# Kernel tuning notes

Measured on AMD Instinct MI355X. Metric: run time of the kernel, lower is better.

Reference implementation:

```python
import jax, jax.numpy as jnp
import numpy as np

B, N_C, N_T, D, DF = 16, 2048, 1024, 2, 2
K, E_OBS = 16, 4
H, DH = 4, 16
F = H * DH  # 64-dim node features (embed_all output)


def setup_inputs() -> dict:
    key = jax.random.key(0)
    ks = jax.random.split(key, 16)
    r = lambda i, shape: jax.random.normal(ks[i], shape, jnp.float32) * 0.05
    d_in = E_OBS + D + DF  # obs(4) + s(2) + f(2) = 8
    return dict(
        s_ctx=jax.random.normal(ks[0], (B, N_C, D), jnp.float32),
        f_ctx=jax.random.normal(ks[1], (B, N_C, DF), jnp.float32),
        s_test=jax.random.normal(ks[2], (B, N_T, D), jnp.float32),
        emb_obs=r(3, (2, E_OBS)),
        W1=r(4, (d_in, 256)), b1=jnp.zeros((256,), jnp.float32),
        W2=r(5, (256, 128)), b2=jnp.zeros((128,), jnp.float32),
        W3=r(6, (128, F)), b3=jnp.zeros((F,), jnp.float32),
        ln_g=jnp.ones((F,), jnp.float32), ln_b=jnp.zeros((F,), jnp.float32),
        Wg=r(7, (F, F)),
        a_src=r(8, (H, DH)), a_dst=r(9, (H, DH)),
        We=r(10, (D, H)), be=jnp.zeros((H,), jnp.float32),
        H1=r(11, (F, 256)), c1=jnp.zeros((256,), jnp.float32),
        H2=r(12, (256, 64)), c2=jnp.zeros((64,), jnp.float32),
        H3=r(13, (64, 2)), c3=jnp.zeros((2,), jnp.float32),
    )


def _knn(q, ctx, k):
    # q [B,Nq,D], ctx [B,Nc,D] -> neighbor indices [B,Nq,K] and displacement edge feats [B,Nq,K,D]
    d2 = (jnp.sum(q * q, -1)[:, :, None] + jnp.sum(ctx * ctx, -1)[:, None, :]
          - 2.0 * jnp.einsum('bqd,bcd->bqc', q, ctx))
    _, idx = jax.lax.top_k(-d2, k)
    nb = jax.vmap(lambda c, i: c[i])(ctx, idx)  # gather neighbor coords per batch
    return idx, q[:, :, None, :] - nb


def _mlp3(x, W1, b1, W2, b2, W3, b3):
    x = jax.nn.gelu(x @ W1 + b1)
    x = jax.nn.gelu(x @ W2 + b2)
    return x @ W3 + b3


def _ln(x, g, b):
    mu = jnp.mean(x, -1, keepdims=True)
    v = jnp.var(x, -1, keepdims=True)
    return (x - mu) * jax.lax.rsqrt(v + 1e-6) * g + b


def reference(s_ctx, f_ctx, s_test, emb_obs, W1, b1, W2, b2, W3, b3, ln_g, ln_b,
              Wg, a_src, a_dst, We, be, H1, c1, H2, c2, H3, c3):
    # --- build kNN graph (ctx->ctx and ctx->test edges, K per receiver) ---
    s_cc, d_cc = _knn(s_ctx, s_ctx, K)
    s_ct, d_ct = _knn(s_test, s_ctx, K)
    edges = jnp.concatenate([d_cc.reshape(-1, D), d_ct.reshape(-1, D)], axis=0)  # [E, D]
    off = (jnp.arange(B) * N_C)[:, None, None]
    senders = jnp.concatenate([(s_cc + off).reshape(-1), (s_ct + off).reshape(-1)])  # [E]
    # receivers == repeat(arange(N), K): edges are grouped K-per-node in node order.

    # --- node embedding: [obs_embed | s | f] -> MLP -> LayerNorm ---
    ctx_in = jnp.concatenate([jnp.broadcast_to(emb_obs[1], (B, N_C, E_OBS)), s_ctx, f_ctx], -1)
    test_in = jnp.concatenate([jnp.broadcast_to(emb_obs[0], (B, N_T, E_OBS)), s_test,
                               jnp.zeros((B, N_T, DF), s_test.dtype)], -1)
    n_ctx = _ln(_mlp3(ctx_in, W1, b1, W2, b2, W3, b3), ln_g, ln_b)
    n_test = _ln(_mlp3(test_in, W1, b1, W2, b2, W3, b3), ln_g, ln_b)
    nodes = jnp.concatenate([n_ctx.reshape(B * N_C, F), n_test.reshape(B * N_T, F)], 0)
    N = B * (N_C + N_T)

    # --- edge-biased GAT message passing (K incoming edges per node) ---
    xp = (nodes @ Wg).reshape(N, H, DH)
    msg = xp[senders].reshape(N, K, H, DH)  # gather sender features
    sc = (jnp.einsum('nkhd,hd->nkh', msg, a_src)
          + jnp.einsum('nhd,hd->nh', xp, a_dst)[:, None, :])
    sc = jax.nn.leaky_relu(sc, 0.2) + (edges @ We + be).reshape(N, K, H)  # edge bias
    alpha = jax.nn.softmax(sc, axis=1)  # softmax over the K neighbors
    out = jnp.einsum('nkh,nkhd->nhd', alpha, msg).reshape(N, F)
    nodes = nodes + out  # residual

    # --- head on test nodes + diagonal MVN output ---
    n_t = nodes[-B * N_T:].reshape(B, N_T, F)
    o = jax.nn.gelu(n_t @ H1 + c1)
    o = jax.nn.gelu(o @ H2 + c2)
    o = o @ H3 + c3  # [B, N_t, 2]
    mean = o[..., 0:1]
    scale = jax.nn.softplus(o[..., 1:2])
    return jnp.concatenate([mean, scale], -1)
```

## Files before the change

kernel.cpp:

```cpp
#include <hip/hip_runtime.h>
#include <math.h>

#define NB 16
#define NCTX 2048
#define NTEST 1024
#define NCTX_TOT (NB*NCTX)
#define NTEST_TOT (NB*NTEST)
#define NTOT (NCTX_TOT + NTEST_TOT)

typedef _Float16 half8 __attribute__((ext_vector_type(8)));
typedef _Float16 half4 __attribute__((ext_vector_type(4)));
typedef float f32x4 __attribute__((ext_vector_type(4)));

__device__ __forceinline__ float gelu_f(float x) {
  float x3 = x * x * x;
  float y = 0.7978845608028654f * fmaf(0.044715f, x3, x);
  float e = __expf(2.0f * y);
  float th = 1.0f - 2.0f * __builtin_amdgcn_rcpf(e + 1.0f);
  return 0.5f * x * (1.0f + th);
}

__device__ __forceinline__ void fma4(float4& a, float s, float4 w) {
  a.x = fmaf(s, w.x, a.x);
  a.y = fmaf(s, w.y, a.y);
  a.z = fmaf(s, w.z, a.z);
  a.w = fmaf(s, w.w, a.w);
}

__device__ __forceinline__ float4 ldg4(const float* p) {
  return *reinterpret_cast<const float4*>(p);
}

__device__ __forceinline__ unsigned fkey(float f) {
  unsigned u = __float_as_uint(f);
  return (u & 0x80000000u) ? ~u : (u ^ 0x80000000u);
}
__device__ __forceinline__ float unfkey(unsigned k) {
  return (k & 0x80000000u) ? __uint_as_float(k ^ 0x80000000u)
                           : __uint_as_float(~k);
}

__global__ __launch_bounds__(256, 3) void knn_prep_kernel(
    const float* __restrict__ s_ctx, const float* __restrict__ s_test,
    int* __restrict__ senders,
    const float* __restrict__ W1, const float* __restrict__ b1,
    const float* __restrict__ emb,
    const float* __restrict__ W2, const float* __restrict__ W3,
    const float* __restrict__ Wg,
    const float* __restrict__ H1, const float* __restrict__ H2,
    _Float16* __restrict__ W2P, _Float16* __restrict__ W3P,
    _Float16* __restrict__ WgP,
    _Float16* __restrict__ H1P, _Float16* __restrict__ H2P,
    float* __restrict__ ctype)
{
  __shared__ __align__(16) unsigned long long sk[4][128];
  const int blk = blockIdx.x;

  if (blk < 40) {
    const int t = blk*256 + (int)threadIdx.x;
    if (t < 4096) {
      int i = t;
      int j = i >> 9, ks = (i >> 6) & 7, l = i & 63;
      int col = 16*j + (l & 15);
      int k0  = ks*32 + (l >> 4)*8;
      half8 o;
      #pragma unroll
      for (int e = 0; e < 8; ++e) o[e] = (_Float16)W2[(k0 + e)*128 + col];
      *reinterpret_cast<half8*>(&W2P[(size_t)i*8]) = o;
    } else if (t < 5120) {
      int i = t - 4096;
      int j = i >> 8, ks = (i >> 6) & 3, l = i & 63;
      int col = 16*j + (l & 15);
      int k0  = ks*32 + (l >> 4)*8;
      half8 o;
      #pragma unroll
      for (int e = 0; e < 8; ++e) o[e] = (_Float16)W3[(k0 + e)*64 + col];
      *reinterpret_cast<half8*>(&W3P[(size_t)i*8]) = o;
    } else if (t < 5632) {
      int i = t - 5120;
      int j = i >> 7, ks = (i >> 6) & 1, l = i & 63;
      int col = 16*j + (l & 15);
      int k0  = ks*32 + (l >> 4)*8;
      half8 o;
      #pragma unroll
      for (int e = 0; e < 8; ++e) o[e] = (_Float16)Wg[(k0 + e)*64 + col];
      *reinterpret_cast<half8*>(&WgP[(size_t)i*8]) = o;
    } else if (t < 7680) {
      int i = t - 5632;
      int j = i >> 7, ks = (i >> 6) & 1, l = i & 63;
      int col = 16*j + (l & 15);
      int k0  = ks*32 + (l >> 4)*8;
      half8 o;
      #pragma unroll
      for (int e = 0; e < 8; ++e) o[e] = (_Float16)H1[(k0 + e)*256 + col];
      *reinterpret_cast<half8*>(&H1P[(size_t)i*8]) = o;
    } else if (t < 9728) {
      int i = t - 7680;
      int j = i >> 9, ks = (i >> 6) & 7, l = i & 63;
      int col = 16*j + (l & 15);
      int k0  = ks*32 + (l >> 4)*8;
      half8 o;
      #pragma unroll
      for (int e = 0; e < 8; ++e) o[e] = (_Float16)H2[(k0 + e)*64 + col];
      *reinterpret_cast<half8*>(&H2P[(size_t)i*8]) = o;
    } else {
      int i = t - 9728;
      int ty = i >> 8, c = i & 255;
      float acc = b1[c];
      #pragma unroll
      for (int k = 0; k < 4; ++k) acc = fmaf(emb[ty*4 + k], W1[k*256 + c], acc);
      ctype[i] = acc;
    }
    return;
  }

  const int t    = threadIdx.x;
  const int lane = t & 63;
  const int w    = t >> 6;
  const int b0   = blk - 40;
  const int unit = (b0 & 7)*512 + (b0 >> 3);
  const int bb   = unit >> 8;
  const int q    = (unit & 255) * 4 + w;
  const int trow = bb * NTEST + q;

  const float* cb = s_ctx + (size_t)bb * NCTX * 2;
  const float qx = s_test[(size_t)trow*2];
  const float qy = s_test[(size_t)trow*2 + 1];
  const float qq = __fadd_rn(__fmul_rn(qx,qx), __fmul_rn(qy,qy));

  float2 p[32];
  #pragma unroll
  for (int it = 0; it < 32; ++it)
    p[it] = *reinterpret_cast<const float2*>(&cb[2*(it*64 + lane)]);

  float d[32];
  float mn = 3.4e38f;
  #pragma unroll
  for (int it = 0; it < 32; ++it) {
    float ss  = __fadd_rn(__fmul_rn(p[it].x,p[it].x), __fmul_rn(p[it].y,p[it].y));
    float dot = __fadd_rn(__fmul_rn(qx, p[it].x), __fmul_rn(qy, p[it].y));
    float d2  = __fsub_rn(__fadd_rn(qq, ss), __fmul_rn(2.0f, dot));
    d[it] = d2;
    mn = fminf(mn, d2);
  }

  unsigned v = fkey(mn);
  #pragma unroll
  for (int k = 2; k <= 64; k <<= 1) {
    #pragma unroll
    for (int j = k >> 1; j >= 1; j >>= 1) {
      unsigned pv = (unsigned)__shfl_xor((int)v, j);
      bool up      = ((lane & k) == 0);
      bool lowHalf = ((lane & j) == 0);
      bool keepMin = (lowHalf == up);
      unsigned mnv = v < pv ? v : pv;
      unsigned mxv = v < pv ? pv : v;
      v = keepMin ? mnv : mxv;
    }
  }
  const float Tf = unfkey((unsigned)__shfl((int)v, 15));

  int cnt = 0;
  #pragma unroll
  for (int it = 0; it < 32; ++it) cnt += (int)(d[it] <= Tf);
  int inc = cnt;
  #pragma unroll
  for (int o = 1; o < 64; o <<= 1) {
    int y = __shfl_up(inc, o);
    if (lane >= o) inc += y;
  }
  const int S = __shfl(inc, 63);
  int pos = inc - cnt;
  #pragma unroll
  for (int it = 0; it < 32; ++it) {
    if (d[it] <= Tf) {
      if (pos < 128)
        sk[w][pos] = ((unsigned long long)fkey(d[it]) << 32)
                   | (unsigned)(it*64 + lane);
      ++pos;
    }
  }

  if (S <= 32) {
    if (lane >= S && lane < 32) sk[w][lane] = ~0ULL;
    unsigned long long pm = sk[w][lane & 31];
    unsigned long long kv[32];
    #pragma unroll
    for (int j = 0; j < 32; ++j) kv[j] = sk[w][j];
    int r0 = 0;
    #pragma unroll
    for (int j = 0; j < 32; ++j)
      r0 += (int)(kv[j] < pm);
    if (lane < S && r0 < 16)
      senders[(size_t)trow*16 + r0] = bb*NCTX + (int)(pm & 0xFFFFFFFFu);
  } else if (S <= 128) {
    unsigned long long p0 = (lane      < S) ? sk[w][lane]      : ~0ULL;
    unsigned long long p1 = (lane + 64 < S) ? sk[w][lane + 64] : ~0ULL;
    int r0 = 0, r1 = 0;
    for (int j = 0; j < S; ++j) {
      unsigned long long kj = sk[w][j];
      r0 += (int)(kj < p0);
      r1 += (int)(kj < p1);
    }
    if (lane < S && r0 < 16)
      senders[(size_t)trow*16 + r0] = bb*NCTX + (int)(p0 & 0xFFFFFFFFu);
    if (lane + 64 < S && r1 < 16)
      senders[(size_t)trow*16 + r1] = bb*NCTX + (int)(p1 & 0xFFFFFFFFu);
  } else {
    if (lane == 0) {
      float dist[16]; int ind[16];
      #pragma unroll
      for (int j=0;j<16;++j){ dist[j]=3.4e38f; ind[j]=0; }
      for (int c = 0; c < NCTX; ++c) {
        float2 pp = *reinterpret_cast<const float2*>(&cb[2*c]);
        float ss  = __fadd_rn(__fmul_rn(pp.x,pp.x), __fmul_rn(pp.y,pp.y));
        float dot = __fadd_rn(__fmul_rn(qx, pp.x), __fmul_rn(qy, pp.y));
        float d2  = __fsub_rn(__fadd_rn(qq, ss), __fmul_rn(2.0f, dot));
        if (d2 < dist[15]) {
          float dj = d2; int ij = c;
          #pragma unroll
          for (int j = 0; j < 16; ++j) {
            bool sw = dj < dist[j];
            float td = dist[j]; int ti = ind[j];
            dist[j] = sw ? dj : td;  ind[j] = sw ? ij : ti;
            dj = sw ? td : dj;       ij = sw ? ti : ij;
          }
        }
      }
      for (int j = 0; j < 16; ++j)
        senders[(size_t)trow*16 + j] = bb*NCTX + ind[j];
    }
  }
}

__global__ __launch_bounds__(256, 4) void mlp_kernel(
    const float* __restrict__ s_ctx, const float* __restrict__ f_ctx,
    const float* __restrict__ s_test,
    const float* __restrict__ ctype, const float* __restrict__ W1,
    const _Float16* __restrict__ W2P, const float* __restrict__ b2,
    const _Float16* __restrict__ W3P, const float* __restrict__ b3,
    const float* __restrict__ ln_g, const float* __restrict__ ln_b,
    const _Float16* __restrict__ WgP,
    const float* __restrict__ a_src, const float* __restrict__ a_dst,
    float* __restrict__ nodes, _Float16* __restrict__ xph,
    float* __restrict__ xps, float* __restrict__ xpd)
{
  __shared__ __align__(16) char smem[34816];
  const int t    = threadIdx.x;
  const int lane = t & 63;
  const int w    = t >> 6;
  const int id   = blockIdx.x;
  char* slice = smem + w * 8704;
  _Float16* h1t  = reinterpret_cast<_Float16*>(slice);
  float (*xin)[4] = reinterpret_cast<float(*)[4]>(slice + 8448);
  _Float16* h2   = h1t;
  _Float16* nodh = h1t + 16*136;
  const int cn = lane & 15;
  const int kg = lane >> 4;
  const int m0 = (id*4 + w) * 16;
  const bool is_ctx = (m0 < NCTX_TOT);

  const _Float16* bQ2 = W2P + lane*8;
  const _Float16* bQ3 = W3P + lane*8;
  const _Float16* bQg = WgP + lane*8;

  half8 bb2[8];
  #pragma unroll
  for (int j = 0; j < 8; ++j)
    bb2[j] = *reinterpret_cast<const half8*>(bQ2 + j*4096);

  {
    int r = lane >> 2, c = lane & 3;
    int n = m0 + r;
    float v;
    if (is_ctx) v = (c < 2) ? s_ctx[2*(size_t)n + c] : f_ctx[2*(size_t)n + (c-2)];
    else { int tn = n - NCTX_TOT; v = (c < 2) ? s_test[2*(size_t)tn + c] : 0.f; }
    xin[r][c] = v;
  }

  {
    const int c0 = lane * 4;
    float4 w4 = ldg4(&W1[4*256 + c0]);
    float4 w5 = ldg4(&W1[5*256 + c0]);
    float4 w6 = ldg4(&W1[6*256 + c0]);
    float4 w7 = ldg4(&W1[7*256 + c0]);
    float4 cbv = ldg4(&ctype[(is_ctx ? 256 : 0) + c0]);
    #pragma unroll
    for (int r = 0; r < 16; ++r) {
      float4 xi = *reinterpret_cast<const float4*>(&xin[r][0]);
      float4 a = cbv;
      fma4(a, xi.x, w4); fma4(a, xi.y, w5);
      fma4(a, xi.z, w6); fma4(a, xi.w, w7);
      half4 o = { (_Float16)gelu_f(a.x), (_Float16)gelu_f(a.y),
                  (_Float16)gelu_f(a.z), (_Float16)gelu_f(a.w) };
      *reinterpret_cast<half4*>(&h1t[r*264 + c0]) = o;
    }
  }

  {
    f32x4 acc[8];
    #pragma unroll
    for (int j = 0; j < 8; ++j) {
      float bv = b2[16*j + cn];
      acc[j] = (f32x4){bv, bv, bv, bv};
    }
    const _Float16* aP = h1t + cn*264 + kg*8;
    #pragma unroll
    for (int ks = 0; ks < 8; ++ks) {
      half8 a = *reinterpret_cast<const half8*>(aP + ks*32);
      half8 bn[8];
      if (ks < 7) {
        #pragma unroll
        for (int j = 0; j < 8; ++j)
          bn[j] = *reinterpret_cast<const half8*>(bQ2 + j*4096 + (ks+1)*512);
      }
      #pragma unroll
      for (int j = 0; j < 8; ++j)
        acc[j] = __builtin_amdgcn_mfma_f32_16x16x32_f16(a, bb2[j], acc[j], 0, 0, 0);
      if (ks < 7) {
        #pragma unroll
        for (int j = 0; j < 8; ++j) bb2[j] = bn[j];
      }
    }
    #pragma unroll
    for (int j = 0; j < 8; ++j)
      #pragma unroll
      for (int r = 0; r < 4; ++r) {
        int m = kg*4 + r;
        h2[m*136 + 16*j + cn] = (_Float16)gelu_f(acc[j][r]);
      }
  }

  {
    f32x4 acc[4];
    #pragma unroll
    for (int j = 0; j < 4; ++j) {
      float bv = b3[16*j + cn];
      acc[j] = (f32x4){bv, bv, bv, bv};
    }
    const _Float16* aP = h2 + cn*136 + kg*8;
    half8 bb[4];
    #pragma unroll
    for (int j = 0; j < 4; ++j)
      bb[j] = *reinterpret_cast<const half8*>(bQ3 + j*2048);
    #pragma unroll
    for (int ks = 0; ks < 4; ++ks) {
      half8 a = *reinterpret_cast<const half8*>(aP + ks*32);
      half8 bn[4];
      if (ks < 3) {
        #pragma unroll
        for (int j = 0; j < 4; ++j)
          bn[j] = *reinterpret_cast<const half8*>(bQ3 + j*2048 + (ks+1)*512);
      }
      #pragma unroll
      for (int j = 0; j < 4; ++j)
        acc[j] = __builtin_amdgcn_mfma_f32_16x16x32_f16(a, bb[j], acc[j], 0, 0, 0);
      if (ks < 3) {
        #pragma unroll
        for (int j = 0; j < 4; ++j) bb[j] = bn[j];
      }
    }
    float gv[4], bvv[4];
    #pragma unroll
    for (int j = 0; j < 4; ++j) { gv[j] = ln_g[16*j+cn]; bvv[j] = ln_b[16*j+cn]; }
    const bool is_test = !is_ctx;
    #pragma unroll
    for (int r = 0; r < 4; ++r) {
      float sv = 0.f, sq = 0.f;
      #pragma unroll
      for (int j = 0; j < 4; ++j) {
        float v = acc[j][r];
        sv += v; sq += v*v;
      }
      #pragma unroll
      for (int o = 1; o < 16; o <<= 1) {
        sv += __shfl_xor(sv, o);
        sq += __shfl_xor(sq, o);
      }
      float mean = sv * (1.0f/64.0f);
      float var  = sq * (1.0f/64.0f) - mean*mean;
      float rstd = rsqrtf(var + 1e-6f);
      int m = kg*4 + r;
      #pragma unroll
      for (int j = 0; j < 4; ++j) {
        float v = (acc[j][r] - mean) * rstd * gv[j] + bvv[j];
        nodh[m*72 + 16*j + cn] = (_Float16)v;
        if (is_test)
          nodes[(size_t)(m0 + m)*64 + 16*j + cn] = v;
      }
    }
  }

  {
    f32x4 acc[4];
    #pragma unroll
    for (int j = 0; j < 4; ++j) acc[j] = (f32x4){0.f, 0.f, 0.f, 0.f};
    const _Float16* aP = nodh + cn*72 + kg*8;
    half8 bg0[4], bg1[4];
    #pragma unroll
    for (int j = 0; j < 4; ++j) {
      bg0[j] = *reinterpret_cast<const half8*>(bQg + j*1024);
      bg1[j] = *reinterpret_cast<const half8*>(bQg + j*1024 + 512);
    }
    half8 a0 = *reinterpret_cast<const half8*>(aP);
    half8 a1 = *reinterpret_cast<const half8*>(aP + 32);
    #pragma unroll
    for (int j = 0; j < 4; ++j)
      acc[j] = __builtin_amdgcn_mfma_f32_16x16x32_f16(a0, bg0[j], acc[j], 0, 0, 0);
    #pragma unroll
    for (int j = 0; j < 4; ++j)
      acc[j] = __builtin_amdgcn_mfma_f32_16x16x32_f16(a1, bg1[j], acc[j], 0, 0, 0);
    #pragma unroll
    for (int r = 0; r < 4; ++r) {
      int m = kg*4 + r;
      #pragma unroll
      for (int j = 0; j < 4; ++j)
        xph[(size_t)(m0 + m)*64 + 16*j + cn] = (_Float16)acc[j][r];
    }
    const float* av = is_ctx ? a_src : a_dst;
    float av0 = av[cn], av1 = av[16+cn], av2 = av[32+cn], av3 = av[48+cn];
    #pragma unroll
    for (int r = 0; r < 4; ++r) {
      float p0 = acc[0][r]*av0, p1 = acc[1][r]*av1;
      float p2 = acc[2][r]*av2, p3 = acc[3][r]*av3;
      #pragma unroll
      for (int o = 1; o < 16; o <<= 1) {
        p0 += __shfl_xor(p0, o); p1 += __shfl_xor(p1, o);
        p2 += __shfl_xor(p2, o); p3 += __shfl_xor(p3, o);
      }
      if (cn == 0) {
        int m = kg*4 + r;
        float4 v = make_float4(p0, p1, p2, p3);
        if (is_ctx)
          *reinterpret_cast<float4*>(&xps[(size_t)(m0 + m)*4]) = v;
        else
          *reinterpret_cast<float4*>(&xpd[(size_t)(m0 + m - NCTX_TOT)*4]) = v;
      }
    }
  }
}

__global__ __launch_bounds__(256, 4) void back_kernel(
    const float* __restrict__ s_ctx, const float* __restrict__ s_test,
    const _Float16* __restrict__ xph, const int* __restrict__ senders,
    const float* __restrict__ xps, const float* __restrict__ xpd,
    const float* __restrict__ We, const float* __restrict__ be,
    const float* __restrict__ nodes,
    const _Float16* __restrict__ H1P, const float* __restrict__ c1,
    const _Float16* __restrict__ H2P, const float* __restrict__ c2,
    const float* __restrict__ H3, const float* __restrict__ c3,
    float* __restrict__ outp)
{
  __shared__ __align__(16) _Float16 xinh[16*72];
  __shared__ __align__(16) _Float16 h1[16*264];
  __shared__ float pp[4][16][2];
  const int tid  = threadIdx.x;
  const int lane = tid & 63;
  const int wv   = tid >> 6;
  const int cn   = lane & 15;
  const int kg   = lane >> 4;
  const int bid  = blockIdx.x;
  const int L    = (bid & 7)*128 + (bid >> 3);
  const int row0 = L * 16;

  {
    const int h  = kg;
    const int kk = cn;
    const int hb = lane & 48;
    const float we0 = We[h], we1 = We[4+h], beh = be[h];
    for (int rr = 0; rr < 4; ++rr) {
      const int rl   = wv*4 + rr;
      const int trow = row0 + rl;
      int s = senders[(size_t)trow*16 + kk];
      s = (s < 0) ? 0 : ((s >= NCTX_TOT) ? NCTX_TOT - 1 : s);
      float pre = xps[(size_t)s*4 + h] + xpd[(size_t)trow*4 + h];
      float lr  = pre >= 0.f ? pre : 0.2f * pre;
      const float qx = s_test[(size_t)trow*2];
      const float qy = s_test[(size_t)trow*2 + 1];
      float ex = qx - s_ctx[(size_t)s*2];
      float ey = qy - s_ctx[(size_t)s*2 + 1];
      float sc = lr + fmaf(ex, we0, fmaf(ey, we1, beh));
      float mx = sc;
      #pragma unroll
      for (int o = 1; o < 16; o <<= 1) mx = fmaxf(mx, __shfl_xor(mx, o));
      float e = __expf(sc - mx);
      float sum = e;
      #pragma unroll
      for (int o = 1; o < 16; o <<= 1) sum += __shfl_xor(sum, o);
      float alpha = e / sum;
      float outv = 0.f;
      #pragma unroll
      for (int k = 0; k < 16; ++k) {
        int   sk = __shfl(s, k);
        float al = __shfl(alpha, hb + k);
        outv = fmaf(al, (float)xph[(size_t)sk*64 + lane], outv);
      }
      float xv = nodes[(size_t)(NCTX_TOT + trow)*64 + lane] + outv;
      xinh[rl*72 + lane] = (_Float16)xv;
    }
  }

  __syncthreads();

  {
    const _Float16* aP  = xinh + cn*72 + kg*8;
    const _Float16* bQ1 = H1P + lane*8;
    half8 a0 = *reinterpret_cast<const half8*>(aP);
    half8 a1 = *reinterpret_cast<const half8*>(aP + 32);
    f32x4 acc[4];
    #pragma unroll
    for (int j2 = 0; j2 < 4; ++j2) {
      const int jj = wv*4 + j2;
      float bv = c1[16*jj + cn];
      acc[j2] = (f32x4){bv, bv, bv, bv};
    }
    half8 b0[4], b1[4];
    #pragma unroll
    for (int j2 = 0; j2 < 4; ++j2) {
      const int jj = wv*4 + j2;
      b0[j2] = *reinterpret_cast<const half8*>(bQ1 + (jj*2 + 0)*512);
      b1[j2] = *reinterpret_cast<const half8*>(bQ1 + (jj*2 + 1)*512);
    }
    #pragma unroll
    for (int j2 = 0; j2 < 4; ++j2)
      acc[j2] = __builtin_amdgcn_mfma_f32_16x16x32_f16(a0, b0[j2], acc[j2], 0, 0, 0);
    #pragma unroll
    for (int j2 = 0; j2 < 4; ++j2)
      acc[j2] = __builtin_amdgcn_mfma_f32_16x16x32_f16(a1, b1[j2], acc[j2], 0, 0, 0);
    #pragma unroll
    for (int j2 = 0; j2 < 4; ++j2) {
      const int jj = wv*4 + j2;
      #pragma unroll
      for (int r = 0; r < 4; ++r)
        h1[(kg*4 + r)*264 + 16*jj + cn] = (_Float16)gelu_f(acc[j2][r]);
    }
  }

  __syncthreads();

  {
    f32x4 acc;
    {
      float bv = c2[16*wv + cn];
      acc = (f32x4){bv, bv, bv, bv};
    }
    const _Float16* aP  = h1 + cn*264 + kg*8;
    const _Float16* bQ2 = H2P + lane*8;
    half8 bb = *reinterpret_cast<const half8*>(bQ2 + wv*4096);
    #pragma unroll
    for (int ks = 0; ks < 8; ++ks) {
      half8 a = *reinterpret_cast<const half8*>(aP + ks*32);
      half8 bn;
      if (ks < 7)
        bn = *reinterpret_cast<const half8*>(bQ2 + wv*4096 + (ks+1)*512);
      acc = __builtin_amdgcn_mfma_f32_16x16x32_f16(a, bb, acc, 0, 0, 0);
      if (ks < 7) bb = bn;
    }
    float h30 = H3[(16*wv + cn)*2 + 0];
    float h31 = H3[(16*wv + cn)*2 + 1];
    #pragma unroll
    for (int r = 0; r < 4; ++r) {
      float g  = gelu_f(acc[r]);
      float p0 = g * h30;
      float p1 = g * h31;
      #pragma unroll
      for (int o = 1; o < 16; o <<= 1) {
        p0 += __shfl_xor(p0, o);
        p1 += __shfl_xor(p1, o);
      }
      if (cn == 0) {
        pp[wv][kg*4 + r][0] = p0;
        pp[wv][kg*4 + r][1] = p1;
      }
    }
  }

  __syncthreads();

  if (wv == 0 && lane < 16) {
    const float c30 = c3[0], c31 = c3[1];
    float m  = pp[0][lane][0] + pp[1][lane][0] + pp[2][lane][0]
             + pp[3][lane][0] + c30;
    float sa = pp[0][lane][1] + pp[1][lane][1] + pp[2][lane][1]
             + pp[3][lane][1] + c31;
    float sv = fmaxf(sa, 0.f) + log1pf(__expf(-fabsf(sa)));
    int row = row0 + lane;
    outp[(size_t)row*2 + 0] = m;
    outp[(size_t)row*2 + 1] = sv;
  }
}

extern "C" void kernel_launch(void* const* d_in, const int* in_sizes, int n_in,
                              void* d_out, int out_size, void* d_ws, size_t ws_size,
                              hipStream_t stream) {
  const float* s_ctx  = (const float*)d_in[0];
  const float* f_ctx  = (const float*)d_in[1];
  const float* s_test = (const float*)d_in[2];
  const float* emb    = (const float*)d_in[3];
  const float* W1 = (const float*)d_in[4];
  const float* b1 = (const float*)d_in[5];
  const float* W2 = (const float*)d_in[6];
  const float* b2 = (const float*)d_in[7];
  const float* W3 = (const float*)d_in[8];
  const float* b3 = (const float*)d_in[9];
  const float* ln_g = (const float*)d_in[10];
  const float* ln_b = (const float*)d_in[11];
  const float* Wg = (const float*)d_in[12];
  const float* a_src = (const float*)d_in[13];
  const float* a_dst = (const float*)d_in[14];
  const float* We = (const float*)d_in[15];
  const float* be = (const float*)d_in[16];
  const float* H1 = (const float*)d_in[17];
  const float* c1 = (const float*)d_in[18];
  const float* H2 = (const float*)d_in[19];
  const float* c2 = (const float*)d_in[20];
  const float* H3 = (const float*)d_in[21];
  const float* c3 = (const float*)d_in[22];

  float* nodes   = (float*)d_ws;
  _Float16* xph  = (_Float16*)(nodes + (size_t)NTOT*64);
  int*   senders = (int*)(xph + (size_t)NTOT*64);
  _Float16* W2P  = (_Float16*)(senders + (size_t)NTEST_TOT*16);
  _Float16* W3P  = W2P + 32768;
  _Float16* WgP  = W3P + 8192;
  _Float16* H1P  = WgP + 4096;
  _Float16* H2P  = H1P + 16384;
  float*   ctype = (float*)(H2P + 16384);
  float*   xps   = ctype + 512;
  float*   xpd   = xps + (size_t)NCTX_TOT*4;
  float* outp    = (float*)d_out;

  hipLaunchKernelGGL(knn_prep_kernel, dim3(4136), dim3(256), 0, stream,
                     s_ctx, s_test, senders,
                     W1, b1, emb, W2, W3, Wg, H1, H2,
                     W2P, W3P, WgP, H1P, H2P, ctype);
  hipLaunchKernelGGL(mlp_kernel, dim3(768), dim3(256), 0, stream,
                     s_ctx, f_ctx, s_test, ctype, W1,
                     W2P, b2, W3P, b3, ln_g, ln_b, WgP,
                     a_src, a_dst, nodes, xph, xps, xpd);
  hipLaunchKernelGGL(back_kernel, dim3(1024), dim3(256), 0, stream,
                     s_ctx, s_test, xph, senders, xps, xpd, We, be,
                     nodes, H1P, c1, H2P, c2, H3, c3, outp);
}
```

Baseline: 61.78 us.

## Stage MLP weight fragments in shared memory shared by all block waves

Each of the four waves used to load its own copy of the W2/W3/Wg MFMA B-fragments from global memory into registers, with manual prefetch. Now the block loads these fragments once into a 16 KB LDS staging buffer, in four chunks for W2 and once each for W3 and Wg, and every wave reads its B operands from LDS. This cuts redundant global and L2 traffic and register pressure. In exchange it adds block-wide barriers, serializes load and compute, uses more LDS, and lowers the launch-bounds occupancy hint from 4 to 3 blocks.

```diff
diff --git a/kernel.cpp b/kernel.cpp
--- a/kernel.cpp
+++ b/kernel.cpp
@@ -233,7 +233,7 @@
   }
 }
 
-__global__ __launch_bounds__(256, 4) void mlp_kernel(
+__global__ __launch_bounds__(256, 3) void mlp_kernel(
     const float* __restrict__ s_ctx, const float* __restrict__ f_ctx,
     const float* __restrict__ s_test,
     const float* __restrict__ ctype, const float* __restrict__ W1,
@@ -246,6 +246,7 @@
     float* __restrict__ xps, float* __restrict__ xpd)
 {
   __shared__ __align__(16) char smem[34816];
+  __shared__ __align__(16) _Float16 stg[8192];
   const int t    = threadIdx.x;
   const int lane = t & 63;
   const int w    = t >> 6;
@@ -260,15 +261,6 @@
   const int m0 = (id*4 + w) * 16;
   const bool is_ctx = (m0 < NCTX_TOT);
 
-  const _Float16* bQ2 = W2P + lane*8;
-  const _Float16* bQ3 = W3P + lane*8;
-  const _Float16* bQg = WgP + lane*8;
-
-  half8 bb2[8];
-  #pragma unroll
-  for (int j = 0; j < 8; ++j)
-    bb2[j] = *reinterpret_cast<const half8*>(bQ2 + j*4096);
-
   {
     int r = lane >> 2, c = lane & 3;
     int n = m0 + r;
@@ -305,21 +297,27 @@
       acc[j] = (f32x4){bv, bv, bv, bv};
     }
     const _Float16* aP = h1t + cn*264 + kg*8;
-    #pragma unroll
-    for (int ks = 0; ks < 8; ++ks) {
-      half8 a = *reinterpret_cast<const half8*>(aP + ks*32);
-      half8 bn[8];
-      if (ks < 7) {
+    for (int r4 = 0; r4 < 4; ++r4) {
+      __syncthreads();
+      #pragma unroll
+      for (int u = 0; u < 4; ++u) {
+        int uu = u*256 + t;
+        int k  = uu >> 6;
+        int o  = (uu & 63) * 8;
+        int j  = k >> 1, kk = k & 1;
+        *reinterpret_cast<half8*>(&stg[k*512 + o]) =
+          *reinterpret_cast<const half8*>(&W2P[(size_t)(j*8 + 2*r4 + kk)*512 + o]);
+      }
+      __syncthreads();
+      #pragma unroll
+      for (int kk = 0; kk < 2; ++kk) {
+        const int ks = 2*r4 + kk;
+        half8 a = *reinterpret_cast<const half8*>(aP + ks*32);
         #pragma unroll
-        for (int j = 0; j < 8; ++j)
-          bn[j] = *reinterpret_cast<const half8*>(bQ2 + j*4096 + (ks+1)*512);
-      }
-      #pragma unroll
-      for (int j = 0; j < 8; ++j)
-        acc[j] = __builtin_amdgcn_mfma_f32_16x16x32_f16(a, bb2[j], acc[j], 0, 0, 0);
-      if (ks < 7) {
-        #pragma unroll
-        for (int j = 0; j < 8; ++j) bb2[j] = bn[j];
+        for (int j = 0; j < 8; ++j) {
+          half8 b = *reinterpret_cast<const half8*>(&stg[(j*2 + kk)*512 + lane*8]);
+          acc[j] = __builtin_amdgcn_mfma_f32_16x16x32_f16(a, b, acc[j], 0, 0, 0);
+        }
       }
     }
     #pragma unroll
@@ -332,6 +330,16 @@
   }
 
   {
+    __syncthreads();
+    #pragma unroll
+    for (int u = 0; u < 4; ++u) {
+      int uu = u*256 + t;
+      int o  = uu * 8;
+      *reinterpret_cast<half8*>(&stg[o]) =
+        *reinterpret_cast<const half8*>(&W3P[o]);
+    }
+    __syncthreads();
+
     f32x4 acc[4];
     #pragma unroll
     for (int j = 0; j < 4; ++j) {
@@ -339,25 +347,13 @@
       acc[j] = (f32x4){bv, bv, bv, bv};
     }
     const _Float16* aP = h2 + cn*136 + kg*8;
-    half8 bb[4];
-    #pragma unroll
-    for (int j = 0; j < 4; ++j)
-      bb[j] = *reinterpret_cast<const half8*>(bQ3 + j*2048);
     #pragma unroll
     for (int ks = 0; ks < 4; ++ks) {
       half8 a = *reinterpret_cast<const half8*>(aP + ks*32);
-      half8 bn[4];
-      if (ks < 3) {
-        #pragma unroll
-        for (int j = 0; j < 4; ++j)
-          bn[j] = *reinterpret_cast<const half8*>(bQ3 + j*2048 + (ks+1)*512);
-      }
-      #pragma unroll
-      for (int j = 0; j < 4; ++j)
-        acc[j] = __builtin_amdgcn_mfma_f32_16x16x32_f16(a, bb[j], acc[j], 0, 0, 0);
-      if (ks < 3) {
-        #pragma unroll
-        for (int j = 0; j < 4; ++j) bb[j] = bn[j];
+      #pragma unroll
+      for (int j = 0; j < 4; ++j) {
+        half8 b = *reinterpret_cast<const half8*>(&stg[(j*4 + ks)*512 + lane*8]);
+        acc[j] = __builtin_amdgcn_mfma_f32_16x16x32_f16(a, b, acc[j], 0, 0, 0);
       }
     }
     float gv[4], bvv[4];
@@ -392,24 +388,32 @@
   }
 
   {
+    __syncthreads();
+    #pragma unroll
+    for (int u = 0; u < 2; ++u) {
+      int uu = u*256 + t;
+      int o  = uu * 8;
+      *reinterpret_cast<half8*>(&stg[o]) =
+        *reinterpret_cast<const half8*>(&WgP[o]);
+    }
+    __syncthreads();
+
     f32x4 acc[4];
     #pragma unroll
     for (int j = 0; j < 4; ++j) acc[j] = (f32x4){0.f, 0.f, 0.f, 0.f};
     const _Float16* aP = nodh + cn*72 + kg*8;
-    half8 bg0[4], bg1[4];
-    #pragma unroll
-    for (int j = 0; j < 4; ++j) {
-      bg0[j] = *reinterpret_cast<const half8*>(bQg + j*1024);
-      bg1[j] = *reinterpret_cast<const half8*>(bQg + j*1024 + 512);
-    }
     half8 a0 = *reinterpret_cast<const half8*>(aP);
     half8 a1 = *reinterpret_cast<const half8*>(aP + 32);
     #pragma unroll
-    for (int j = 0; j < 4; ++j)
-      acc[j] = __builtin_amdgcn_mfma_f32_16x16x32_f16(a0, bg0[j], acc[j], 0, 0, 0);
-    #pragma unroll
-    for (int j = 0; j < 4; ++j)
-      acc[j] = __builtin_amdgcn_mfma_f32_16x16x32_f16(a1, bg1[j], acc[j], 0, 0, 0);
+    for (int j = 0; j < 4; ++j) {
+      half8 b = *reinterpret_cast<const half8*>(&stg[(j*2 + 0)*512 + lane*8]);
+      acc[j] = __builtin_amdgcn_mfma_f32_16x16x32_f16(a0, b, acc[j], 0, 0, 0);
+    }
+    #pragma unroll
+    for (int j = 0; j < 4; ++j) {
+      half8 b = *reinterpret_cast<const half8*>(&stg[(j*2 + 1)*512 + lane*8]);
+      acc[j] = __builtin_amdgcn_mfma_f32_16x16x32_f16(a1, b, acc[j], 0, 0, 0);
+    }
     #pragma unroll
     for (int r = 0; r < 4; ++r) {
       int m = kg*4 + r;
```

After: 62.53 us. Within noise of the previous version (+1.2%).
